# Optimization experiments

Measured on AMD Instinct MI355X. Metric: run time of the kernel, lower is better.

Reference implementation:

```python
import jax, jax.numpy as jnp
import numpy as np

WEIGHT_SCALE = 0.01  # keep exp(rowsum*colsum) numerically sane


def setup_inputs() -> dict:
    key = jax.random.key(0)
    k1, k2 = jax.random.split(key)
    T, C, D = 4096, 64, 512
    x = jax.random.normal(k1, (T, D), dtype=jnp.float32)
    weight = jax.random.normal(k2, (C, D), dtype=jnp.float32) * WEIGHT_SCALE
    return {"x": x, "weight": weight}


def _softreorder(inp_colsums, weight):
    # softreorder_elementwise: exp(sum(outer(u, v))) == exp(sum(u) * sum(v)).
    # det_i = sum_d exp(rowsum(W)_i * colsum(inp)_d); nom_ij = exp(rowsum(W)_i * colsum(W)_j)
    rs = jnp.sum(weight, axis=1)            # (C,) row sums of weight
    cs = jnp.sum(weight, axis=0)            # (D,) column sums of weight
    det = jnp.sum(jnp.exp(rs[:, None] * inp_colsums[None, :]), axis=1)  # (C,)
    nom = jnp.exp(rs[:, None] * cs[None, :])                            # (C, D)
    return nom / det[:, None]


def reference(x, weight):
    T = x.shape[0]
    C, D = weight.shape
    # forward feeds emb[t] = zeros into softreorder, so inp column sums are all zero
    zero_colsums = jnp.zeros((D,), dtype=weight.dtype)
    remap = _softreorder(zero_colsums, weight)           # (C, D), identical for all t
    return jnp.broadcast_to(remap[None, :, :], (T, C, D))
```

## Files before the change

### kernel.cpp

```cpp
#include <hip/hip_runtime.h>


#define T_DIM 4096
#define C_DIM 64
#define D_DIM 512

typedef float f32x4 __attribute__((ext_vector_type(4)));

__global__ __launch_bounds__(256) void fused_broadcast_kernel(
    const float* __restrict__ w, f32x4* __restrict__ out) {
    const int t = threadIdx.x;
    const unsigned b = blockIdx.x;
    const unsigned tid = b * 256u + t;

    const int c0 = (int)((b & 31u) * 2u);
    const int c1 = c0 + 1;
    const int dbase = (4 * t) & (D_DIM - 1);

    float p0 = w[c0 * D_DIM + t] + w[c0 * D_DIM + 256 + t];
    float p1 = w[c1 * D_DIM + t] + w[c1 * D_DIM + 256 + t];
    #pragma unroll
    for (int off = 32; off > 0; off >>= 1) {
        p0 += __shfl_down(p0, off);
        p1 += __shfl_down(p1, off);
    }
    __shared__ float red[8];
    const int wave = t >> 6, lane = t & 63;
    if (lane == 0) { red[wave * 2] = p0; red[wave * 2 + 1] = p1; }
    __syncthreads();
    const float rs0 = (red[0] + red[2]) + (red[4] + red[6]);
    const float rs1 = (red[1] + red[3]) + (red[5] + red[7]);
    const float rs = (t >> 7) ? rs1 : rs0;

    const f32x4* col = (const f32x4*)(w + dbase);
    f32x4 a0 = {0.f, 0.f, 0.f, 0.f}, a1 = a0, a2 = a0, a3 = a0;
    #pragma unroll
    for (int r = 0; r < C_DIM; r += 4) {
        a0 += col[(r + 0) * (D_DIM / 4)];
        a1 += col[(r + 1) * (D_DIM / 4)];
        a2 += col[(r + 2) * (D_DIM / 4)];
        a3 += col[(r + 3) * (D_DIM / 4)];
    }
    const f32x4 cs4 = (a0 + a1) + (a2 + a3);

    const float inv_det = 1.0f / (float)D_DIM;
    f32x4 v;
    v.x = expf(rs * cs4.x) * inv_det;
    v.y = expf(rs * cs4.y) * inv_det;
    v.z = expf(rs * cs4.z) * inv_det;
    v.w = expf(rs * cs4.w) * inv_det;

    const unsigned STRIDE = 256u * 256u;
    const int ITERS = (T_DIM * C_DIM * D_DIM / 4) / STRIDE;
    f32x4* p = out + tid;
    #pragma unroll 4
    for (int i = 0; i < ITERS; ++i) {
        *p = v;
        p += STRIDE;
    }
}

extern "C" void kernel_launch(void* const* d_in, const int* in_sizes, int n_in,
                              void* d_out, int out_size, void* d_ws, size_t ws_size,
                              hipStream_t stream) {
    const float* weight = (const float*)d_in[1];
    fused_broadcast_kernel<<<256, 256, 0, stream>>>(weight, (f32x4*)d_out);
}
```

Baseline: 98.79 us.

## Compute full row/col sums in shared memory, widen per-thread stores, use nontemporal writes

Each block now computes all column sums and all row sums of the weight into shared memory instead of a per-block partial reduction via shuffles. The store mapping changes so each wave writes two contiguous C rows (four vectors per thread per iteration), with 128 iterations over a larger stride. Stores use nontemporal builtins to avoid polluting caches on the 512MB broadcast write. The cost is more redundant weight reads per block and a different write-interleaving pattern.

```diff
diff --git a/kernel.cpp b/kernel.cpp
--- a/kernel.cpp
+++ b/kernel.cpp
@@ -6,56 +6,71 @@
 #define D_DIM 512
 
 typedef float f32x4 __attribute__((ext_vector_type(4)));
+typedef float f32x2 __attribute__((ext_vector_type(2)));
 
 __global__ __launch_bounds__(256) void fused_broadcast_kernel(
     const float* __restrict__ w, f32x4* __restrict__ out) {
     const int t = threadIdx.x;
     const unsigned b = blockIdx.x;
-    const unsigned tid = b * 256u + t;
+    const int wv = t >> 6, l = t & 63;
 
-    const int c0 = (int)((b & 31u) * 2u);
-    const int c1 = c0 + 1;
-    const int dbase = (4 * t) & (D_DIM - 1);
+    __shared__ f32x2 cs2[D_DIM / 2];
+    __shared__ float rs[C_DIM];
 
-    float p0 = w[c0 * D_DIM + t] + w[c0 * D_DIM + 256 + t];
-    float p1 = w[c1 * D_DIM + t] + w[c1 * D_DIM + 256 + t];
-    #pragma unroll
-    for (int off = 32; off > 0; off >>= 1) {
-        p0 += __shfl_down(p0, off);
-        p1 += __shfl_down(p1, off);
+    {
+        const f32x2* w2 = (const f32x2*)w;
+        f32x2 a0 = {0.f, 0.f}, a1 = a0, a2 = a0, a3 = a0;
+        #pragma unroll
+        for (int r = 0; r < C_DIM; r += 4) {
+            a0 += w2[(r + 0) * 256 + t];
+            a1 += w2[(r + 1) * 256 + t];
+            a2 += w2[(r + 2) * 256 + t];
+            a3 += w2[(r + 3) * 256 + t];
+        }
+        cs2[t] = (a0 + a1) + (a2 + a3);
     }
-    __shared__ float red[8];
-    const int wave = t >> 6, lane = t & 63;
-    if (lane == 0) { red[wave * 2] = p0; red[wave * 2 + 1] = p1; }
+    if (t < C_DIM) {
+        const f32x4* wr = (const f32x4*)(w + t * D_DIM);
+        f32x4 a0 = {0.f, 0.f, 0.f, 0.f}, a1 = a0, a2 = a0, a3 = a0;
+        #pragma unroll
+        for (int i = 0; i < 128; i += 4) {
+            a0 += wr[i + 0];
+            a1 += wr[i + 1];
+            a2 += wr[i + 2];
+            a3 += wr[i + 3];
+        }
+        f32x4 s = (a0 + a1) + (a2 + a3);
+        rs[t] = (s.x + s.y) + (s.z + s.w);
+    }
     __syncthreads();
-    const float rs0 = (red[0] + red[2]) + (red[4] + red[6]);
-    const float rs1 = (red[1] + red[3]) + (red[5] + red[7]);
-    const float rs = (t >> 7) ? rs1 : rs0;
 
-    const f32x4* col = (const f32x4*)(w + dbase);
-    f32x4 a0 = {0.f, 0.f, 0.f, 0.f}, a1 = a0, a2 = a0, a3 = a0;
-    #pragma unroll
-    for (int r = 0; r < C_DIM; r += 4) {
-        a0 += col[(r + 0) * (D_DIM / 4)];
-        a1 += col[(r + 1) * (D_DIM / 4)];
-        a2 += col[(r + 2) * (D_DIM / 4)];
-        a3 += col[(r + 3) * (D_DIM / 4)];
-    }
-    const f32x4 cs4 = (a0 + a1) + (a2 + a3);
+    const int c0 = (int)(b & 7u) * 8 + wv * 2;
+    const float r0 = rs[c0], r1 = rs[c0 + 1];
+    const f32x4* cs4 = (const f32x4*)cs2;
+    const f32x4 csA = cs4[l], csB = cs4[64 + l];
 
     const float inv_det = 1.0f / (float)D_DIM;
-    f32x4 v;
-    v.x = expf(rs * cs4.x) * inv_det;
-    v.y = expf(rs * cs4.y) * inv_det;
-    v.z = expf(rs * cs4.z) * inv_det;
-    v.w = expf(rs * cs4.w) * inv_det;
+    auto remap4 = [inv_det](float r, f32x4 c) {
+        f32x4 o;
+        o.x = expf(r * c.x) * inv_det;
+        o.y = expf(r * c.y) * inv_det;
+        o.z = expf(r * c.z) * inv_det;
+        o.w = expf(r * c.w) * inv_det;
+        return o;
+    };
+    const f32x4 v0 = remap4(r0, csA);
+    const f32x4 v1 = remap4(r0, csB);
+    const f32x4 v2 = remap4(r1, csA);
+    const f32x4 v3 = remap4(r1, csB);
 
-    const unsigned STRIDE = 256u * 256u;
-    const int ITERS = (T_DIM * C_DIM * D_DIM / 4) / STRIDE;
-    f32x4* p = out + tid;
+    const unsigned STRIDE = 262144u;
+    f32x4* p = out + (size_t)b * 1024 + (size_t)wv * 256 + l;
     #pragma unroll 4
-    for (int i = 0; i < ITERS; ++i) {
-        *p = v;
+    for (int i = 0; i < 128; ++i) {
+        __builtin_nontemporal_store(v0, p);
+        __builtin_nontemporal_store(v1, p + 64);
+        __builtin_nontemporal_store(v2, p + 128);
+        __builtin_nontemporal_store(v3, p + 192);
         p += STRIDE;
     }
 }
```

New measurement: 104.7 us. +6.0%, slower.
